# Kernel tuning notes

Hardware: AMD Instinct MI355X
Metric: run time of the kernel (lower is better)

## Reference

```python
import jax, jax.numpy as jnp
import numpy as np

R = 4          # args.search_range
D = 2 * R + 1  # window size per axis -> D*D = 81 output channels


def setup_inputs() -> dict:
    key = jax.random.key(0)
    k1, k2 = jax.random.split(key)
    B, C, H, W = 4, 128, 64, 128
    src = jax.random.normal(k1, (B, C, H, W), dtype=jnp.float32)
    tgt = jax.random.normal(k2, (B, C, H, W), dtype=jnp.float32)
    return {"src": src, "tgt": tgt}


def reference(src, tgt):
    # Faithful to the torch code: tgt is zero-padded by R on each spatial side,
    # then for output pixel (i, j) the window indices into the PADDED tensor are
    # I in [i-R, i+R], J in [j-R, j+R]. For i < R the index is negative, which in
    # torch wraps around -> reproduce with modular indexing.
    B, C, H, W = src.shape
    tp = jnp.pad(tgt, ((0, 0), (0, 0), (R, R), (R, R)))  # [B,C,H+2R,W+2R]
    Hp, Wp = H + 2 * R, W + 2 * R
    # col_idx[dj, j] = (j - R + dj) mod Wp
    col_idx = (jnp.arange(W)[None, :] - R + jnp.arange(D)[:, None]) % Wp  # [D,W]
    outs = []
    for di in range(D):  # small fixed loop over 9 row offsets
        row_idx = (jnp.arange(H) - R + di) % Hp        # [H]
        t_rows = tp[:, :, row_idx, :]                  # [B,C,H,Wp]
        t_win = t_rows[:, :, :, col_idx]               # [B,C,H,D,W]
        # channel-dot-product per pixel and per column offset
        outs.append(jnp.einsum('bchdw,bchw->bdhw', t_win, src))
    # channel ordering k = di*D + dj matches the original double loop over (I, J)
    return jnp.concatenate(outs, axis=1)  # [B, D*D, H, W]
```

## Files before the change

### kernel.cpp

```cpp
#include <hip/hip_runtime.h>
#include <stdint.h>

#define NB 4
#define NC 128
#define NH 64
#define NW 128
#define HW (NH * NW)
#define ND 9
#define NOUT (ND * ND)
#define SH 4
#define QW 32
#define TROW 392
#define SROW 264
#define OTILE (ND * 32)

typedef __attribute__((ext_vector_type(8))) short short8;
typedef __attribute__((ext_vector_type(4))) float f32x4;

__device__ __forceinline__ ushort f2bf(float f) {
  uint u = __float_as_uint(f);
  u += 0x7FFFu + ((u >> 16) & 1u);
  return (ushort)(u >> 16);
}

__global__ __launch_bounds__(576, 1) void costvol_kernel(const float* __restrict__ src,
                                                         const float* __restrict__ tgt,
                                                         float* __restrict__ out) {
  __shared__ ushort tgtS[9][16 * TROW];
  __shared__ ushort srcS[SH][16 * SROW];
  __shared__ float  outlds[ND * OTILE];

  const int tid  = threadIdx.x;
  const int lane = tid & 63;
  const int wave = tid >> 6;
  const int col  = lane & 15;
  const int g    = lane >> 4;

  const int xcd   = blockIdx.x & 7;
  const int r     = blockIdx.x >> 3;
  const int combo = ((r >> 4) << 3) | xcd;
  const int b     = combo >> 2;
  const int q     = combo & 3;
  const int h0    = (r & 15) << 2;

  const float* sb = src + (size_t)(b * NC) * HW;
  const float* tb = tgt + (size_t)(b * NC) * HW;

  for (int cell = tid; cell < SH * 128; cell += 576) {
    const int hh = cell >> 7;
    const int cc = cell & 127;
    const int fc = cc & 7;
    const int o  = cc >> 3;
    const float* p = sb + (size_t)(h0 + hh) * NW + q * QW + 4 * fc + (size_t)(o * 8) * HW;
    float4 v[8];
#pragma unroll
    for (int j = 0; j < 8; ++j) v[j] = *(const float4*)(p + (size_t)j * HW);
    ushort* d = srcS[hh] + o * SROW + (4 * fc) * 8;
#pragma unroll
    for (int i = 0; i < 4; ++i) {
      short8 e;
#pragma unroll
      for (int j = 0; j < 8; ++j) e[j] = (short)f2bf(((const float*)&v[j])[i]);
      *(short8*)&d[i * 8] = e;
    }
  }
  {
    const int y0  = (h0 >= 8) ? h0 - 8 : 0;
    const int nts = h0 - y0 + 1;
    for (int cell = tid; cell < nts * 192; cell += 576) {
      const int y  = y0 + cell / 192;
      const int cc = cell % 192;
      const int fc = cc % 12;
      const int o  = cc / 12;
      const int g0 = q * QW - 16 + 4 * fc;
      const float* p = tb + (size_t)y * NW + (g0 < 0 ? 0 : g0) + (size_t)(o * 8) * HW;
      float4 v[8];
#pragma unroll
      for (int j = 0; j < 8; ++j) v[j] = *(const float4*)(p + (size_t)j * HW);
      ushort* d = tgtS[y % 9] + o * TROW + (4 * fc) * 8;
#pragma unroll
      for (int i = 0; i < 4; ++i) {
        short8 e;
#pragma unroll
        for (int j = 0; j < 8; ++j) e[j] = (short)f2bf(((const float*)&v[j])[i]);
        *(short8*)&d[i * 8] = e;
      }
    }
  }
  __syncthreads();

  for (int hh = 0; hh < SH; ++hh) {
    const int h = h0 + hh;

    float4 pv[8];
    const bool hs = (hh < SH - 1) && (tid < 192);
    int sfc = 0, so = 0;
    if (hs) {
      sfc = tid % 12;
      so  = tid / 12;
      const int g0 = q * QW - 16 + 4 * sfc;
      const float* p = tb + (size_t)(h + 1) * NW + (g0 < 0 ? 0 : g0) + (size_t)(so * 8) * HW;
#pragma unroll
      for (int j = 0; j < 8; ++j) pv[j] = *(const float4*)(p + (size_t)j * HW);
    }

    const int y = h + wave - 8;
    if (y >= 0) {
      const ushort* Bp = tgtS[y % 9];
      const ushort* Ap = srcS[hh];
      f32x4 aD0 = {0.f,0.f,0.f,0.f}, aS0 = {0.f,0.f,0.f,0.f};
      f32x4 aD1 = {0.f,0.f,0.f,0.f}, aS1 = {0.f,0.f,0.f,0.f};
#pragma unroll
      for (int kk = 0; kk < 4; ++kk) {
        const int ro = 4 * kk + g;
        const short8 A0 = *(const short8*)&Ap[ro * SROW + col * 8];
        const short8 A1 = *(const short8*)&Ap[ro * SROW + (16 + col) * 8];
        const short8 B0 = *(const short8*)&Bp[ro * TROW + col * 8];
        const short8 B1 = *(const short8*)&Bp[ro * TROW + (16 + col) * 8];
        const short8 B2 = *(const short8*)&Bp[ro * TROW + (32 + col) * 8];
        aS0 = __builtin_amdgcn_mfma_f32_16x16x32_bf16(A0, B0, aS0, 0, 0, 0);
        aD0 = __builtin_amdgcn_mfma_f32_16x16x32_bf16(A0, B1, aD0, 0, 0, 0);
        aS1 = __builtin_amdgcn_mfma_f32_16x16x32_bf16(A1, B1, aS1, 0, 0, 0);
        aD1 = __builtin_amdgcn_mfma_f32_16x16x32_bf16(A1, B2, aD1, 0, 0, 0);
      }
      float* ol = &outlds[wave * OTILE];
#pragma unroll
      for (int qr = 0; qr < 4; ++qr) {
        const int row = 4 * g + qr;
        const int djd = col - row + 8;
        const int djs = col - row - 8;
        if (djd >= 0 && djd <= 8) {
          ol[djd * 32 + ((row + 4 * djd) & 31)]      = aD0[qr];
          ol[djd * 32 + ((16 + row + 4 * djd) & 31)] = aD1[qr];
        }
        if (djs >= 0 && djs <= 8) {
          ol[djs * 32 + ((row + 4 * djs) & 31)]      = aS0[qr];
          ol[djs * 32 + ((16 + row + 4 * djs) & 31)] = aS1[qr];
        }
      }
    }
    __syncthreads();

    for (int s = tid; s < ND * ND * 8; s += 576) {
      const int di = s / 72;
      const int rr = s % 72;
      const int dj = rr >> 3;
      const int w4 = (rr & 7) << 2;
      f32x4 o = *(const f32x4*)&outlds[di * OTILE + dj * 32 + ((w4 + 4 * dj) & 31)];
      const bool vb = (h + di - 8) >= 0;
      const int wg = q * QW + w4;
#pragma unroll
      for (int i = 0; i < 4; ++i)
        if (!vb || (wg + i + dj < 8)) o[i] = 0.f;
      *(f32x4*)(out + ((size_t)((b * NOUT + di * ND + dj) * NH + h)) * NW + wg) = o;
    }

    if (hs) {
      ushort* d = tgtS[(h + 1) % 9] + so * TROW + (4 * sfc) * 8;
#pragma unroll
      for (int i = 0; i < 4; ++i) {
        short8 e;
#pragma unroll
        for (int j = 0; j < 8; ++j) e[j] = (short)f2bf(((const float*)&pv[j])[i]);
        *(short8*)&d[i * 8] = e;
      }
    }
    __syncthreads();
  }
}

extern "C" void kernel_launch(void* const* d_in, const int* in_sizes, int n_in,
                              void* d_out, int out_size, void* d_ws, size_t ws_size,
                              hipStream_t stream) {
  const float* src = (const float*)d_in[0];
  const float* tgt = (const float*)d_in[1];
  float* out = (float*)d_out;
  costvol_kernel<<<dim3(256), dim3(576), 0, stream>>>(src, tgt, out);
}
```

Before: 86.08 us.

## Retile to 16-wide by 8-row blocks and skip left-halo MFMAs at q=0

Each block now covers a 16-pixel-wide column strip and 8 rows instead of 32 wide and 4 rows, with a new block-to-(batch, row, column) mapping. The MFMA inner loop is split so the shifted-window product is skipped for the leftmost strip, where those outputs are all zero. Narrower strips cut the shared-memory footprint and the per-row MFMA count, and taller row tiles give more reuse of the 9-row target ring. In exchange, each strip reloads a 16-pixel halo that is now as wide as the strip itself, so redundant target loads go up.

```diff
diff --git a/kernel.cpp b/kernel.cpp
--- a/kernel.cpp
+++ b/kernel.cpp
@@ -8,11 +8,11 @@
 #define HW (NH * NW)
 #define ND 9
 #define NOUT (ND * ND)
-#define SH 4
-#define QW 32
-#define TROW 392
-#define SROW 264
-#define OTILE (ND * 32)
+#define SH 8
+#define QW 16
+#define TROW 264
+#define SROW 136
+#define OTILE (ND * 16)
 
 typedef __attribute__((ext_vector_type(8))) short short8;
 typedef __attribute__((ext_vector_type(4))) float f32x4;
@@ -36,22 +36,22 @@
   const int col  = lane & 15;
   const int g    = lane >> 4;
 
-  const int xcd   = blockIdx.x & 7;
-  const int r     = blockIdx.x >> 3;
-  const int combo = ((r >> 4) << 3) | xcd;
-  const int b     = combo >> 2;
-  const int q     = combo & 3;
-  const int h0    = (r & 15) << 2;
+  const int xcd = blockIdx.x & 7;
+  const int k   = blockIdx.x >> 3;
+  const int b   = xcd >> 1;
+  const int q   = k & 7;
+  const int h0  = ((xcd & 1) << 5) | ((k >> 3) << 3);
+  const int w0  = q * QW;
 
   const float* sb = src + (size_t)(b * NC) * HW;
   const float* tb = tgt + (size_t)(b * NC) * HW;
 
-  for (int cell = tid; cell < SH * 128; cell += 576) {
-    const int hh = cell >> 7;
-    const int cc = cell & 127;
-    const int fc = cc & 7;
-    const int o  = cc >> 3;
-    const float* p = sb + (size_t)(h0 + hh) * NW + q * QW + 4 * fc + (size_t)(o * 8) * HW;
+  for (int cell = tid; cell < SH * 64; cell += 576) {
+    const int hh = cell >> 6;
+    const int cc = cell & 63;
+    const int o  = cc >> 2;
+    const int fc = cc & 3;
+    const float* p = sb + (size_t)(h0 + hh) * NW + w0 + 4 * fc + (size_t)(o * 8) * HW;
     float4 v[8];
 #pragma unroll
     for (int j = 0; j < 8; ++j) v[j] = *(const float4*)(p + (size_t)j * HW);
@@ -67,12 +67,12 @@
   {
     const int y0  = (h0 >= 8) ? h0 - 8 : 0;
     const int nts = h0 - y0 + 1;
-    for (int cell = tid; cell < nts * 192; cell += 576) {
-      const int y  = y0 + cell / 192;
-      const int cc = cell % 192;
-      const int fc = cc % 12;
-      const int o  = cc / 12;
-      const int g0 = q * QW - 16 + 4 * fc;
+    for (int cell = tid; cell < nts * 128; cell += 576) {
+      const int y  = y0 + (cell >> 7);
+      const int cc = cell & 127;
+      const int o  = cc >> 3;
+      const int fc = cc & 7;
+      const int g0 = w0 - 16 + 4 * fc;
       const float* p = tb + (size_t)y * NW + (g0 < 0 ? 0 : g0) + (size_t)(o * 8) * HW;
       float4 v[8];
 #pragma unroll
@@ -93,12 +93,12 @@
     const int h = h0 + hh;
 
     float4 pv[8];
-    const bool hs = (hh < SH - 1) && (tid < 192);
-    int sfc = 0, so = 0;
+    const bool hs = (hh < SH - 1) && (tid < 128);
+    int so = 0, sfc = 0;
     if (hs) {
-      sfc = tid % 12;
-      so  = tid / 12;
-      const int g0 = q * QW - 16 + 4 * sfc;
+      so  = tid >> 3;
+      sfc = tid & 7;
+      const int g0 = w0 - 16 + 4 * sfc;
       const float* p = tb + (size_t)(h + 1) * NW + (g0 < 0 ? 0 : g0) + (size_t)(so * 8) * HW;
 #pragma unroll
       for (int j = 0; j < 8; ++j) pv[j] = *(const float4*)(p + (size_t)j * HW);
@@ -108,47 +108,46 @@
     if (y >= 0) {
       const ushort* Bp = tgtS[y % 9];
       const ushort* Ap = srcS[hh];
-      f32x4 aD0 = {0.f,0.f,0.f,0.f}, aS0 = {0.f,0.f,0.f,0.f};
-      f32x4 aD1 = {0.f,0.f,0.f,0.f}, aS1 = {0.f,0.f,0.f,0.f};
+      short8 A[4], BD[4];
 #pragma unroll
       for (int kk = 0; kk < 4; ++kk) {
         const int ro = 4 * kk + g;
-        const short8 A0 = *(const short8*)&Ap[ro * SROW + col * 8];
-        const short8 A1 = *(const short8*)&Ap[ro * SROW + (16 + col) * 8];
-        const short8 B0 = *(const short8*)&Bp[ro * TROW + col * 8];
-        const short8 B1 = *(const short8*)&Bp[ro * TROW + (16 + col) * 8];
-        const short8 B2 = *(const short8*)&Bp[ro * TROW + (32 + col) * 8];
-        aS0 = __builtin_amdgcn_mfma_f32_16x16x32_bf16(A0, B0, aS0, 0, 0, 0);
-        aD0 = __builtin_amdgcn_mfma_f32_16x16x32_bf16(A0, B1, aD0, 0, 0, 0);
-        aS1 = __builtin_amdgcn_mfma_f32_16x16x32_bf16(A1, B1, aS1, 0, 0, 0);
-        aD1 = __builtin_amdgcn_mfma_f32_16x16x32_bf16(A1, B2, aD1, 0, 0, 0);
+        A[kk]  = *(const short8*)&Ap[ro * SROW + col * 8];
+        BD[kk] = *(const short8*)&Bp[ro * TROW + (16 + col) * 8];
       }
+      f32x4 aD = {0.f, 0.f, 0.f, 0.f};
+      f32x4 aS = {0.f, 0.f, 0.f, 0.f};
+#pragma unroll
+      for (int kk = 0; kk < 4; ++kk)
+        aD = __builtin_amdgcn_mfma_f32_16x16x32_bf16(A[kk], BD[kk], aD, 0, 0, 0);
+      if (q) {
+#pragma unroll
+        for (int kk = 0; kk < 4; ++kk) {
+          const short8 BS = *(const short8*)&Bp[(4 * kk + g) * TROW + col * 8];
+          aS = __builtin_amdgcn_mfma_f32_16x16x32_bf16(A[kk], BS, aS, 0, 0, 0);
+        }
+      }
+
       float* ol = &outlds[wave * OTILE];
 #pragma unroll
       for (int qr = 0; qr < 4; ++qr) {
         const int row = 4 * g + qr;
         const int djd = col - row + 8;
         const int djs = col - row - 8;
-        if (djd >= 0 && djd <= 8) {
-          ol[djd * 32 + ((row + 4 * djd) & 31)]      = aD0[qr];
-          ol[djd * 32 + ((16 + row + 4 * djd) & 31)] = aD1[qr];
-        }
-        if (djs >= 0 && djs <= 8) {
-          ol[djs * 32 + ((row + 4 * djs) & 31)]      = aS0[qr];
-          ol[djs * 32 + ((16 + row + 4 * djs) & 31)] = aS1[qr];
-        }
+        if (djd >= 0 && djd <= 8) ol[djd * 16 + ((row + 4 * djd) & 15)] = aD[qr];
+        if (djs >= 0 && djs <= 8) ol[djs * 16 + ((row + 4 * djs) & 15)] = aS[qr];
       }
     }
     __syncthreads();
 
-    for (int s = tid; s < ND * ND * 8; s += 576) {
-      const int di = s / 72;
-      const int rr = s % 72;
-      const int dj = rr >> 3;
-      const int w4 = (rr & 7) << 2;
-      f32x4 o = *(const f32x4*)&outlds[di * OTILE + dj * 32 + ((w4 + 4 * dj) & 31)];
+    for (int s = tid; s < ND * ND * 4; s += 576) {
+      const int di = s / 36;
+      const int rr = s % 36;
+      const int dj = rr >> 2;
+      const int w4 = (rr & 3) << 2;
+      f32x4 o = *(const f32x4*)&outlds[di * OTILE + dj * 16 + ((w4 + 4 * dj) & 15)];
       const bool vb = (h + di - 8) >= 0;
-      const int wg = q * QW + w4;
+      const int wg = w0 + w4;
 #pragma unroll
       for (int i = 0; i < 4; ++i)
         if (!vb || (wg + i + dj < 8)) o[i] = 0.f;
```

Result: no change. 87.01 us (+1.1%).
